# Optimization experiments

Hardware: AMD Instinct MI355X
Metric: run time of the kernel (lower is better)

Reference implementation:

```python
import jax, jax.numpy as jnp
import numpy as np

FP8_MAX = 448.0  # float8_e4m3fn max
EPS = 1e-6
H = 4096
T = 16384


def _rmsnorm(x, w, eps=EPS):
    # vLLM RMSNorm: x * rsqrt(mean(x^2) + eps) * weight, computed in fp32
    ms = jnp.mean(x * x, axis=-1, keepdims=True)
    return x * jax.lax.rsqrt(ms + eps) * w


def _fp8_linear_dyn(y, w_t, wscale):
    # per-token dynamic fp8 quant: scale = max|y| / 448, quantize, fp8 GEMM, dequant
    s = jnp.max(jnp.abs(y), axis=-1, keepdims=True) / FP8_MAX  # [T,1]
    s = jnp.maximum(s, 1e-10)
    q = jnp.clip(y / s, -FP8_MAX, FP8_MAX)
    q = q.astype(jnp.float8_e4m3fn).astype(jnp.float32)  # snap to fp8 grid
    out = q @ w_t                                         # [T,H]
    return out * s * wscale[:, 0]                          # per-token * per-out-channel


def setup_inputs() -> dict:
    key = jax.random.key(0)
    ks = jax.random.split(key, 9)
    x = jax.random.uniform(ks[0], (T, H), dtype=jnp.float32)
    # RMSNorm weights (init ones in vLLM; perturb for a nontrivial baseline)
    nw0 = 1.0 + 0.1 * jax.random.normal(ks[1], (H,), dtype=jnp.float32)
    nw1 = 1.0 + 0.1 * jax.random.normal(ks[2], (H,), dtype=jnp.float32)
    nw2 = 1.0 + 0.1 * jax.random.normal(ks[3], (H,), dtype=jnp.float32)
    # fp8 weights: rand(H,H) snapped to e4m3 grid, transposed (y @ W.T)
    def fp8_w(k):
        w = jax.random.uniform(k, (H, H), dtype=jnp.float32)
        return w.astype(jnp.float8_e4m3fn).astype(jnp.float32).T
    w0 = fp8_w(ks[4])
    w1 = fp8_w(ks[5])
    ws0 = jax.random.uniform(ks[6], (H, 1), dtype=jnp.float32)
    ws1 = jax.random.uniform(ks[7], (H, 1), dtype=jnp.float32)
    return {"x": x, "nw0": nw0, "nw1": nw1, "nw2": nw2,
            "w0": w0, "w1": w1, "ws0": ws0, "ws1": ws1}


def reference(x, nw0, nw1, nw2, w0, w1, ws0, ws1):
    resid = jnp.sqrt(x)
    y = _rmsnorm(x, nw0)
    x2 = _fp8_linear_dyn(y, w0, ws0)
    # fused add + rmsnorm: residual updated in place semantics
    resid = x2 + resid
    y2 = _rmsnorm(resid, nw1)
    x3 = _fp8_linear_dyn(y2, w1, ws1)
    resid = x3 + resid
    y3 = _rmsnorm(resid, nw2)
    return y3
```

## Files before the change

kernel.cpp:

```cpp
#include <hip/hip_runtime.h>
#include <stdint.h>

#define TT 16384
#define HH 4096

typedef uint8_t u8;
typedef uint32_t u32;
typedef __attribute__((ext_vector_type(16))) float f32x16;
typedef __attribute__((ext_vector_type(8))) int i32x8;

__device__ __forceinline__ u32 cvt4_fp8(float a, float b, float c, float d) {
  u32 v = 0;
  v = __builtin_amdgcn_cvt_pk_fp8_f32(a, b, v, false);
  v = __builtin_amdgcn_cvt_pk_fp8_f32(c, d, v, true);
  return v;
}

__device__ __forceinline__ void gl_lds16(const void* g, void* l) {
  __builtin_amdgcn_global_load_lds(
      (const __attribute__((address_space(1))) void*)g,
      (__attribute__((address_space(3))) void*)l, 16, 0, 0);
}

__device__ __forceinline__ i32x8 ld32B(const u8* p0, const u8* p1) {
  const uint4 a = *(const uint4*)p0;
  const uint4 b = *(const uint4*)p1;
  i32x8 r;
  r[0] = (int)a.x; r[1] = (int)a.y; r[2] = (int)a.z; r[3] = (int)a.w;
  r[4] = (int)b.x; r[5] = (int)b.y; r[6] = (int)b.z; r[7] = (int)b.w;
  return r;
}

__global__ __launch_bounds__(256) void kwquant(const float* __restrict__ w,
                                               u8* __restrict__ wq) {
  __shared__ __align__(16) u8 tile[64][68];
  const int n0 = blockIdx.x * 64;
  const int k0 = blockIdx.y * 64;
  const int t = threadIdx.x;
  const int tr = t >> 4, tc = t & 15;
#pragma unroll
  for (int p = 0; p < 4; ++p) {
    const int kl = p * 16 + tr;
    const float4 v = *(const float4*)(w + (size_t)(k0 + kl) * HH + n0 + tc * 4);
    const u32 pk = cvt4_fp8(v.x, v.y, v.z, v.w);
    tile[tc * 4 + 0][kl] = (u8)(pk);
    tile[tc * 4 + 1][kl] = (u8)(pk >> 8);
    tile[tc * 4 + 2][kl] = (u8)(pk >> 16);
    tile[tc * 4 + 3][kl] = (u8)(pk >> 24);
  }
  __syncthreads();
  const int jr = t >> 2;
  const int kc = (t & 3) * 16;
  uint4 ov;
  ov.x = *(const u32*)&tile[jr][kc + 0];
  ov.y = *(const u32*)&tile[jr][kc + 4];
  ov.z = *(const u32*)&tile[jr][kc + 8];
  ov.w = *(const u32*)&tile[jr][kc + 12];
  *(uint4*)(wq + (size_t)(n0 + jr) * HH + k0 + kc) = ov;
}

__device__ __forceinline__ float wred_sum(float v) {
#pragma unroll
  for (int o = 32; o; o >>= 1) v += __shfl_down(v, o, 64);
  return v;
}
__device__ __forceinline__ float wred_max(float v) {
#pragma unroll
  for (int o = 32; o; o >>= 1) v = fmaxf(v, __shfl_down(v, o, 64));
  return v;
}

template <int MODE>
__global__ __launch_bounds__(256) void knorm(const float* __restrict__ src,
                                             const float* __restrict__ nw,
                                             float* __restrict__ resid_out,
                                             u8* __restrict__ qout,
                                             float* __restrict__ sout,
                                             float* __restrict__ yout) {
  __shared__ float red[4];
  __shared__ float redm[4];
  const int row = blockIdx.x;
  const int t = threadIdx.x;
  const int lane = t & 63, wid = t >> 6;
  const float* rp = src + (size_t)row * HH;

  float4 xv[4];
  float ssq = 0.f;
#pragma unroll
  for (int p = 0; p < 4; ++p) {
    xv[p] = *((const float4*)rp + p * 256 + t);
    ssq += xv[p].x * xv[p].x;
    ssq += xv[p].y * xv[p].y;
    ssq += xv[p].z * xv[p].z;
    ssq += xv[p].w * xv[p].w;
  }
  if (MODE == 0) {
    float* rr = resid_out + (size_t)row * HH;
#pragma unroll
    for (int p = 0; p < 4; ++p) {
      float4 r4;
      r4.x = sqrtf(xv[p].x); r4.y = sqrtf(xv[p].y);
      r4.z = sqrtf(xv[p].z); r4.w = sqrtf(xv[p].w);
      *((float4*)rr + p * 256 + t) = r4;
    }
  }
  ssq = wred_sum(ssq);
  if (lane == 0) red[wid] = ssq;
  __syncthreads();
  const float ms = (((red[0] + red[1]) + red[2]) + red[3]) * (1.0f / HH);
  const float inv = 1.0f / sqrtf(ms + 1e-6f);

  float y[16];
  float amax = 0.f;
#pragma unroll
  for (int p = 0; p < 4; ++p) {
    const float4 wv = *((const float4*)nw + p * 256 + t);
    y[p * 4 + 0] = (xv[p].x * inv) * wv.x;
    y[p * 4 + 1] = (xv[p].y * inv) * wv.y;
    y[p * 4 + 2] = (xv[p].z * inv) * wv.z;
    y[p * 4 + 3] = (xv[p].w * inv) * wv.w;
    amax = fmaxf(amax, fabsf(y[p * 4 + 0]));
    amax = fmaxf(amax, fabsf(y[p * 4 + 1]));
    amax = fmaxf(amax, fabsf(y[p * 4 + 2]));
    amax = fmaxf(amax, fabsf(y[p * 4 + 3]));
  }

  if (MODE == 2) {
    float* yp = yout + (size_t)row * HH;
#pragma unroll
    for (int p = 0; p < 4; ++p) {
      float4 o;
      o.x = y[p * 4 + 0]; o.y = y[p * 4 + 1];
      o.z = y[p * 4 + 2]; o.w = y[p * 4 + 3];
      *((float4*)yp + p * 256 + t) = o;
    }
    return;
  }

  amax = wred_max(amax);
  if (lane == 0) redm[wid] = amax;
  __syncthreads();
  const float bmax = fmaxf(fmaxf(redm[0], redm[1]), fmaxf(redm[2], redm[3]));
  const float sval = fmaxf(bmax / 448.0f, 1e-10f);

  u32* qp = (u32*)(qout + (size_t)row * HH);
#pragma unroll
  for (int p = 0; p < 4; ++p) {
    float q0 = fminf(fmaxf(y[p * 4 + 0] / sval, -448.f), 448.f);
    float q1 = fminf(fmaxf(y[p * 4 + 1] / sval, -448.f), 448.f);
    float q2 = fminf(fmaxf(y[p * 4 + 2] / sval, -448.f), 448.f);
    float q3 = fminf(fmaxf(y[p * 4 + 3] / sval, -448.f), 448.f);
    qp[p * 256 + t] = cvt4_fp8(q0, q1, q2, q3);
  }
  if (t == 0) sout[row] = sval;
}

__global__ __launch_bounds__(256) void kgemm(const u8* __restrict__ Aq,
                                             const u8* __restrict__ Bq,
                                             const float* __restrict__ srow,
                                             const float* __restrict__ wsc,
                                             float* __restrict__ resid) {
  constexpr int K = HH, N = HH;
  constexpr int NT = K / 64;
  __shared__ __align__(16) u8 smAf[3 * 128 * 64];
  __shared__ __align__(16) u8 smBf[3 * 128 * 64];

  const int bidraw = blockIdx.x;
  const int xcd = bidraw & 7;
  const int c = bidraw >> 3;
  const int g = c >> 4;
  const int gr = g >> 3, gc = g & 7;
  const int gm = (c >> 2) & 3, gn = c & 3;
  const int tm = xcd * 16 + gr * 4 + gm;
  const int tn = gc * 4 + gn;
  const int row0 = tm * 128, col0 = tn * 128;

  const int t = threadIdx.x;
  const int lane = t & 63, wid = t >> 6;
  const int wr = wid >> 1, wc = wid & 1;
  const int rl32 = lane & 31, hi = lane >> 5;

  f32x16 acc[2][2];
#pragma unroll
  for (int m = 0; m < 2; ++m)
#pragma unroll
    for (int n = 0; n < 2; ++n) acc[m][n] = (f32x16)0.f;

  int aoffg[2], boffg[2], ldso[2];
#pragma unroll
  for (int p = 0; p < 2; ++p) {
    const int off = (wid * 2 + p) * 1024 + lane * 16;
    const int r = off >> 6;
    const int cb = ((off >> 4) & 3) ^ ((r >> 1) & 3);
    aoffg[p] = (row0 + r) * K + cb * 16;
    boffg[p] = (col0 + r) * K + cb * 16;
    ldso[p] = off;
  }

  int aro[2][2], bro[2][2];
#pragma unroll
  for (int m = 0; m < 2; ++m) {
    const int r = wr * 64 + m * 32 + rl32;
    const int swz = (r >> 1) & 3;
    aro[m][0] = r * 64 + ((hi * 2) ^ swz) * 16;
    aro[m][1] = r * 64 + ((hi * 2 + 1) ^ swz) * 16;
  }
#pragma unroll
  for (int n = 0; n < 2; ++n) {
    const int r = wc * 64 + n * 32 + rl32;
    const int swz = (r >> 1) & 3;
    bro[n][0] = r * 64 + ((hi * 2) ^ swz) * 16;
    bro[n][1] = r * 64 + ((hi * 2 + 1) ^ swz) * 16;
  }

#pragma unroll
  for (int p = 0; p < 2; ++p) {
    gl_lds16(Aq + aoffg[p], smAf + ldso[p]);
    gl_lds16(Bq + boffg[p], smBf + ldso[p]);
  }
#pragma unroll
  for (int p = 0; p < 2; ++p) {
    gl_lds16(Aq + aoffg[p] + 64, smAf + 8192 + ldso[p]);
    gl_lds16(Bq + boffg[p] + 64, smBf + 8192 + ldso[p]);
  }
  asm volatile("s_waitcnt vmcnt(4)" ::: "memory");
  __builtin_amdgcn_s_barrier();
  __builtin_amdgcn_sched_barrier(0);

  int bc = 0;
  int bs = 2;
  for (int it = 0; it < NT; ++it) {
    if (it + 2 < NT) {
      const size_t ko = (size_t)(it + 2) * 64;
      u8* dA = smAf + bs * 8192;
      u8* dB = smBf + bs * 8192;
#pragma unroll
      for (int p = 0; p < 2; ++p) {
        gl_lds16(Aq + aoffg[p] + ko, dA + ldso[p]);
        gl_lds16(Bq + boffg[p] + ko, dB + ldso[p]);
      }
    }

    const u8* sA = smAf + bc * 8192;
    const u8* sB = smBf + bc * 8192;
    i32x8 av[2], bv[2];
#pragma unroll
    for (int m = 0; m < 2; ++m) av[m] = ld32B(sA + aro[m][0], sA + aro[m][1]);
#pragma unroll
    for (int n = 0; n < 2; ++n) bv[n] = ld32B(sB + bro[n][0], sB + bro[n][1]);
    __builtin_amdgcn_s_setprio(1);
#pragma unroll
    for (int m = 0; m < 2; ++m)
#pragma unroll
      for (int n = 0; n < 2; ++n)
        acc[m][n] = __builtin_amdgcn_mfma_scale_f32_32x32x64_f8f6f4(
            av[m], bv[n], acc[m][n], 0 , 0 ,
            0, 0x7f7f7f7f, 0, 0x7f7f7f7f);
    __builtin_amdgcn_s_setprio(0);

    if (it + 2 < NT) {
      asm volatile("s_waitcnt vmcnt(4)" ::: "memory");
    } else if (it + 1 < NT) {
      asm volatile("s_waitcnt vmcnt(0)" ::: "memory");
    }
    __builtin_amdgcn_sched_barrier(0);
    __builtin_amdgcn_s_barrier();
    __builtin_amdgcn_sched_barrier(0);

    bc = (bc == 2) ? 0 : bc + 1;
    bs = (bs == 2) ? 0 : bs + 1;
  }

  const int cc = rl32;
  const int rb = hi * 4;
  float wvv[2];
#pragma unroll
  for (int n = 0; n < 2; ++n) wvv[n] = wsc[col0 + wc * 64 + n * 32 + cc];
#pragma unroll
  for (int m = 0; m < 2; ++m) {
#pragma unroll
    for (int g2 = 0; g2 < 4; ++g2) {
#pragma unroll
      for (int j = 0; j < 4; ++j) {
        const int row = row0 + wr * 64 + m * 32 + g2 * 8 + rb + j;
        const float sv = srow[row];
#pragma unroll
        for (int n = 0; n < 2; ++n) {
          const int col = col0 + wc * 64 + n * 32 + cc;
          const size_t idx = (size_t)row * N + col;
          resid[idx] = resid[idx] + (acc[m][n][g2 * 4 + j] * sv) * wvv[n];
        }
      }
    }
  }
}

extern "C" void kernel_launch(void* const* d_in, const int* in_sizes, int n_in,
                              void* d_out, int out_size, void* d_ws, size_t ws_size,
                              hipStream_t stream) {
  const float* x   = (const float*)d_in[0];
  const float* nw0 = (const float*)d_in[1];
  const float* nw1 = (const float*)d_in[2];
  const float* nw2 = (const float*)d_in[3];
  const float* w0  = (const float*)d_in[4];
  const float* w1  = (const float*)d_in[5];
  const float* ws0 = (const float*)d_in[6];
  const float* ws1 = (const float*)d_in[7];
  float* out = (float*)d_out;

  u8* q = (u8*)d_ws;
  u8* w0q = q + (size_t)TT * HH;
  u8* w1q = w0q + (size_t)HH * HH;
  float* sbuf = (float*)(w1q + (size_t)HH * HH);

  dim3 wg(HH / 64, HH / 64);
  kwquant<<<wg, 256, 0, stream>>>(w0, w0q);
  kwquant<<<wg, 256, 0, stream>>>(w1, w1q);

  knorm<0><<<TT, 256, 0, stream>>>(x, nw0, out, q, sbuf, nullptr);
  kgemm<<<(TT / 128) * (HH / 128), 256, 0, stream>>>(q, w0q, sbuf, ws0, out);
  knorm<1><<<TT, 256, 0, stream>>>(out, nw1, nullptr, q, sbuf, nullptr);
  kgemm<<<(TT / 128) * (HH / 128), 256, 0, stream>>>(q, w1q, sbuf, ws1, out);
  knorm<2><<<TT, 256, 0, stream>>>(out, nw2, nullptr, nullptr, nullptr, out);
}
```

Baseline: 1.047 ms.

## Deepen GEMM LDS pipeline to four stages and double-buffer register fragments

The fp8 GEMM main loop moves from a three-slot LDS ring to a four-slot ring, prefetching three K tiles ahead. It also adds register ping-pong: fragments for the next tile are read from LDS while the MFMAs for the current tile run, with the loop unrolled by two. This aims to hide LDS read latency behind MFMA work and keep more global loads in flight. In exchange it uses more LDS (64KB per block), which may lower occupancy, and more VGPRs for the second fragment set. The vmcnt accounting with the deeper prefetch also has to stay correct.

```diff
diff --git a/kernel.cpp b/kernel.cpp
--- a/kernel.cpp
+++ b/kernel.cpp
@@ -162,8 +162,8 @@
                                              float* __restrict__ resid) {
   constexpr int K = HH, N = HH;
   constexpr int NT = K / 64;
-  __shared__ __align__(16) u8 smAf[3 * 128 * 64];
-  __shared__ __align__(16) u8 smBf[3 * 128 * 64];
+  __shared__ __align__(16) u8 smAf[4 * 128 * 64];
+  __shared__ __align__(16) u8 smBf[4 * 128 * 64];
 
   const int bidraw = blockIdx.x;
   const int xcd = bidraw & 7;
@@ -223,52 +223,97 @@
     gl_lds16(Aq + aoffg[p] + 64, smAf + 8192 + ldso[p]);
     gl_lds16(Bq + boffg[p] + 64, smBf + 8192 + ldso[p]);
   }
+#pragma unroll
+  for (int p = 0; p < 2; ++p) {
+    gl_lds16(Aq + aoffg[p] + 128, smAf + 16384 + ldso[p]);
+    gl_lds16(Bq + boffg[p] + 128, smBf + 16384 + ldso[p]);
+  }
   asm volatile("s_waitcnt vmcnt(4)" ::: "memory");
   __builtin_amdgcn_s_barrier();
   __builtin_amdgcn_sched_barrier(0);
 
-  int bc = 0;
-  int bs = 2;
-  for (int it = 0; it < NT; ++it) {
-    if (it + 2 < NT) {
-      const size_t ko = (size_t)(it + 2) * 64;
-      u8* dA = smAf + bs * 8192;
-      u8* dB = smBf + bs * 8192;
-#pragma unroll
-      for (int p = 0; p < 2; ++p) {
-        gl_lds16(Aq + aoffg[p] + ko, dA + ldso[p]);
-        gl_lds16(Bq + boffg[p] + ko, dB + ldso[p]);
-      }
-    }
-
-    const u8* sA = smAf + bc * 8192;
-    const u8* sB = smBf + bc * 8192;
-    i32x8 av[2], bv[2];
-#pragma unroll
-    for (int m = 0; m < 2; ++m) av[m] = ld32B(sA + aro[m][0], sA + aro[m][1]);
-#pragma unroll
-    for (int n = 0; n < 2; ++n) bv[n] = ld32B(sB + bro[n][0], sB + bro[n][1]);
-    __builtin_amdgcn_s_setprio(1);
-#pragma unroll
-    for (int m = 0; m < 2; ++m)
-#pragma unroll
-      for (int n = 0; n < 2; ++n)
-        acc[m][n] = __builtin_amdgcn_mfma_scale_f32_32x32x64_f8f6f4(
-            av[m], bv[n], acc[m][n], 0 , 0 ,
-            0, 0x7f7f7f7f, 0, 0x7f7f7f7f);
-    __builtin_amdgcn_s_setprio(0);
-
-    if (it + 2 < NT) {
-      asm volatile("s_waitcnt vmcnt(4)" ::: "memory");
-    } else if (it + 1 < NT) {
-      asm volatile("s_waitcnt vmcnt(0)" ::: "memory");
-    }
-    __builtin_amdgcn_sched_barrier(0);
-    __builtin_amdgcn_s_barrier();
-    __builtin_amdgcn_sched_barrier(0);
-
-    bc = (bc == 2) ? 0 : bc + 1;
-    bs = (bs == 2) ? 0 : bs + 1;
+  i32x8 av0[2], bv0[2], av1[2], bv1[2];
+#pragma unroll
+  for (int m = 0; m < 2; ++m) av0[m] = ld32B(smAf + aro[m][0], smAf + aro[m][1]);
+#pragma unroll
+  for (int n = 0; n < 2; ++n) bv0[n] = ld32B(smBf + bro[n][0], smBf + bro[n][1]);
+
+  for (int it = 0; it < NT; it += 2) {
+    {
+      const int j = it;
+      if (j + 3 < NT) {
+        const size_t ko = (size_t)(j + 3) * 64;
+        u8* dA = smAf + ((j + 3) & 3) * 8192;
+        u8* dB = smBf + ((j + 3) & 3) * 8192;
+#pragma unroll
+        for (int p = 0; p < 2; ++p) {
+          gl_lds16(Aq + aoffg[p] + ko, dA + ldso[p]);
+          gl_lds16(Bq + boffg[p] + ko, dB + ldso[p]);
+        }
+      }
+      if (j + 1 < NT) {
+        const u8* sA = smAf + ((j + 1) & 3) * 8192;
+        const u8* sB = smBf + ((j + 1) & 3) * 8192;
+#pragma unroll
+        for (int m = 0; m < 2; ++m) av1[m] = ld32B(sA + aro[m][0], sA + aro[m][1]);
+#pragma unroll
+        for (int n = 0; n < 2; ++n) bv1[n] = ld32B(sB + bro[n][0], sB + bro[n][1]);
+      }
+      __builtin_amdgcn_s_setprio(1);
+#pragma unroll
+      for (int m = 0; m < 2; ++m)
+#pragma unroll
+        for (int n = 0; n < 2; ++n)
+          acc[m][n] = __builtin_amdgcn_mfma_scale_f32_32x32x64_f8f6f4(
+              av0[m], bv0[n], acc[m][n], 0 , 0 ,
+              0, 0x7f7f7f7f, 0, 0x7f7f7f7f);
+      __builtin_amdgcn_s_setprio(0);
+      if (j + 3 < NT) {
+        asm volatile("s_waitcnt vmcnt(4)" ::: "memory");
+      } else if (j + 2 < NT) {
+        asm volatile("s_waitcnt vmcnt(0)" ::: "memory");
+      }
+      __builtin_amdgcn_sched_barrier(0);
+      __builtin_amdgcn_s_barrier();
+      __builtin_amdgcn_sched_barrier(0);
+    }
+    {
+      const int j = it + 1;
+      if (j + 3 < NT) {
+        const size_t ko = (size_t)(j + 3) * 64;
+        u8* dA = smAf + ((j + 3) & 3) * 8192;
+        u8* dB = smBf + ((j + 3) & 3) * 8192;
+#pragma unroll
+        for (int p = 0; p < 2; ++p) {
+          gl_lds16(Aq + aoffg[p] + ko, dA + ldso[p]);
+          gl_lds16(Bq + boffg[p] + ko, dB + ldso[p]);
+        }
+      }
+      if (j + 1 < NT) {
+        const u8* sA = smAf + ((j + 1) & 3) * 8192;
+        const u8* sB = smBf + ((j + 1) & 3) * 8192;
+#pragma unroll
+        for (int m = 0; m < 2; ++m) av0[m] = ld32B(sA + aro[m][0], sA + aro[m][1]);
+#pragma unroll
+        for (int n = 0; n < 2; ++n) bv0[n] = ld32B(sB + bro[n][0], sB + bro[n][1]);
+      }
+      __builtin_amdgcn_s_setprio(1);
+#pragma unroll
+      for (int m = 0; m < 2; ++m)
+#pragma unroll
+        for (int n = 0; n < 2; ++n)
+          acc[m][n] = __builtin_amdgcn_mfma_scale_f32_32x32x64_f8f6f4(
+              av1[m], bv1[n], acc[m][n], 0, 0, 0, 0x7f7f7f7f, 0, 0x7f7f7f7f);
+      __builtin_amdgcn_s_setprio(0);
+      if (j + 3 < NT) {
+        asm volatile("s_waitcnt vmcnt(4)" ::: "memory");
+      } else if (j + 2 < NT) {
+        asm volatile("s_waitcnt vmcnt(0)" ::: "memory");
+      }
+      __builtin_amdgcn_sched_barrier(0);
+      __builtin_amdgcn_s_barrier();
+      __builtin_amdgcn_sched_barrier(0);
+    }
   }
 
   const int cc = rl32;
```

New measurement: 1.213 ms. 1.16x slower.
